# Kernel optimization log

Hardware: AMD Instinct MI355X
Metric: run time of the kernel (lower is better)

The kernel has to match this reference:

```python
import jax, jax.numpy as jnp
import numpy as np

N_NODES = 100000
N_EDGES = 1600000
H_FEATS = 128
OUT_CLASSES = 6


def setup_inputs() -> dict:
    key = jax.random.key(0)
    ks = jax.random.split(key, 9)
    h = jax.random.normal(ks[0], (N_NODES, H_FEATS), dtype=jnp.float32)
    src = jax.random.randint(ks[1], (N_EDGES,), 0, N_NODES)
    dst = jax.random.randint(ks[2], (N_EDGES,), 0, N_NODES)
    # torch nn.Linear convention: y = x @ W.T + b, W shape [out, in]
    W1 = jax.random.normal(ks[3], (64, 2 * H_FEATS), dtype=jnp.float32) * 0.05
    b1 = jax.random.normal(ks[4], (64,), dtype=jnp.float32) * 0.05
    W2 = jax.random.normal(ks[5], (32, 64), dtype=jnp.float32) * 0.05
    b2 = jax.random.normal(ks[6], (32,), dtype=jnp.float32) * 0.05
    W3 = jax.random.normal(ks[7], (OUT_CLASSES, 32), dtype=jnp.float32) * 0.05
    b3 = jax.random.normal(ks[8], (OUT_CLASSES,), dtype=jnp.float32) * 0.05
    return {"h": h, "src": src, "dst": dst, "W1": W1, "b1": b1,
            "W2": W2, "b2": b2, "W3": W3, "b3": b3}


def reference(h, src, dst, W1, b1, W2, b2, W3, b3):
    # Per-edge gather of src/dst node features, concat -> [E, 2*H]
    x = jnp.concatenate([h[src], h[dst]], axis=1)
    x = jax.nn.relu(x @ W1.T + b1)   # [E, 64]
    x = jax.nn.relu(x @ W2.T + b2)   # [E, 32]
    return x @ W3.T + b3             # [E, output_class]
```

## Files before the change

kernel.cpp:

```cpp
#include <hip/hip_runtime.h>
#include <hip/hip_bf16.h>
#include <stdint.h>


#define H 128

typedef short bf16x8 __attribute__((ext_vector_type(8)));
typedef float f32x4  __attribute__((ext_vector_type(4)));

__device__ __forceinline__ uint16_t f2bf(float f) {
    uint32_t u = __float_as_uint(f);
    return (uint16_t)((u + 0x7fffu + ((u >> 16) & 1u)) >> 16);
}

__device__ __forceinline__ uint32_t cvtpk(float lo, float hi) {
    uint32_t r;
    asm("v_cvt_pk_bf16_f32 %0, %1, %2" : "=v"(r) : "v"(lo), "v"(hi));
    return r;
}

__device__ __forceinline__ uint32_t bfadd2_relu(uint32_t a, uint32_t b) {
    float alo = __uint_as_float(a << 16);
    float ahi = __uint_as_float(a & 0xffff0000u);
    float blo = __uint_as_float(b << 16);
    float bhi = __uint_as_float(b & 0xffff0000u);
    float slo = fmaxf(alo + blo, 0.f);
    float shi = fmaxf(ahi + bhi, 0.f);
    return cvtpk(slo, shi);
}

__global__ void prep_weights(const float* __restrict__ W1,
                             const float* __restrict__ W2,
                             const float* __restrict__ W3,
                             uint16_t* __restrict__ Bfrag,
                             uint16_t* __restrict__ EFrag)
{
    int t = blockIdx.x * blockDim.x + threadIdx.x;
    int stride = gridDim.x * blockDim.x;
    for (int i = t; i < 4 * 8 * 64 * 8; i += stride) {
        int j    = i & 7;
        int lane = (i >> 3) & 63;
        int nt   = (i >> 9) & 7;
        int kt   = (i >> 12);
        int k = kt * 32 + (lane >> 4) * 8 + j;
        int n = nt * 16 + (lane & 15);
        float v = (n < 64) ? W1[n * 256 + k] : W1[(n - 64) * 256 + 128 + k];
        Bfrag[i] = f2bf(v);
    }
    for (int i = t; i < 5 * 64 * 8; i += stride) {
        int j    = i & 7;
        int lane = (i >> 3) & 63;
        int f    = i >> 9;
        uint16_t v;
        if (f < 4) {
            int kt = f >> 1, nt = f & 1;
            int k = kt * 32 + (lane >> 4) * 8 + j;
            int n = nt * 16 + (lane & 15);
            v = f2bf(W2[n * 64 + k]);
        } else {
            int k = (lane >> 4) * 8 + j;
            int n = lane & 15;
            v = (n < 6) ? f2bf(W3[n * 32 + k]) : (uint16_t)0;
        }
        EFrag[i] = v;
    }
}

__global__ void __launch_bounds__(256) node_gemm(
    const float* __restrict__ h,
    const uint16_t* __restrict__ Bfrag,
    const float* __restrict__ b1,
    uint16_t* __restrict__ pre, int N)
{
    const int wave = threadIdx.x >> 6;
    const int lane = threadIdx.x & 63;
    const int n0 = (blockIdx.x * 4 + wave) * 32;
    if (n0 >= N) return;

    const int m15  = lane & 15;
    const int quad = lane >> 4;

    bf16x8 hb[2][4];
#pragma unroll
    for (int t = 0; t < 2; t++) {
        int row = n0 + t * 16 + m15; if (row >= N) row = N - 1;
        const float* hrow = h + (size_t)row * H + quad * 8;
#pragma unroll
        for (int kt = 0; kt < 4; kt++) {
            float4 lo = *(const float4*)(hrow + kt * 32);
            float4 hi = *(const float4*)(hrow + kt * 32 + 4);
            union { bf16x8 v; uint32_t u[4]; } B;
            B.u[0] = cvtpk(lo.x, lo.y); B.u[1] = cvtpk(lo.z, lo.w);
            B.u[2] = cvtpk(hi.x, hi.y); B.u[3] = cvtpk(hi.z, hi.w);
            hb[t][kt] = B.v;
        }
    }

    const bool ok0 = (n0 + m15) < N;
    const bool ok1 = (n0 + 16 + m15) < N;
    uint16_t* prow0 = pre + (size_t)(n0 + m15) * H;
    uint16_t* prow1 = pre + (size_t)(n0 + 16 + m15) * H;

#pragma unroll
    for (int ct = 0; ct < 8; ct++) {
        f32x4 acc0 = {0.f, 0.f, 0.f, 0.f};
        f32x4 acc1 = {0.f, 0.f, 0.f, 0.f};
#pragma unroll
        for (int kt = 0; kt < 4; kt++) {
            bf16x8 afr = *(const bf16x8*)(Bfrag + ((size_t)(kt * 8 + ct) * 64 + lane) * 8);
            acc0 = __builtin_amdgcn_mfma_f32_16x16x32_bf16(afr, hb[0][kt], acc0, 0, 0, 0);
            acc1 = __builtin_amdgcn_mfma_f32_16x16x32_bf16(afr, hb[1][kt], acc1, 0, 0, 0);
        }
        float4 bv = {0.f, 0.f, 0.f, 0.f};
        if (ct < 4) bv = *(const float4*)(b1 + ct * 16 + quad * 4);
        const int off = ct * 16 + quad * 4;
        if (ok0) {
            uint32_t p0 = cvtpk(acc0[0] + bv.x, acc0[1] + bv.y);
            uint32_t p1 = cvtpk(acc0[2] + bv.z, acc0[3] + bv.w);
            *(uint2*)(prow0 + off) = uint2{p0, p1};
        }
        if (ok1) {
            uint32_t p0 = cvtpk(acc1[0] + bv.x, acc1[1] + bv.y);
            uint32_t p1 = cvtpk(acc1[2] + bv.z, acc1[3] + bv.w);
            *(uint2*)(prow1 + off) = uint2{p0, p1};
        }
    }
}

__global__ void __launch_bounds__(256) edge_mlp(
    const uint16_t* __restrict__ pre,
    const int* __restrict__ src, const int* __restrict__ dst,
    const uint16_t* __restrict__ EFrag,
    const float* __restrict__ b2, const float* __restrict__ b3,
    float* __restrict__ out, long E)
{
    __shared__ uint16_t zbuf[4][64 * 40];

    const int wave = threadIdx.x >> 6;
    const int lane = threadIdx.x & 63;
    const int m15  = lane & 15;
    const int quad = lane >> 4;
    uint16_t* zw = &zbuf[wave][0];

    bf16x8 bL2[4], bL3;
#pragma unroll
    for (int f = 0; f < 4; f++) bL2[f] = *(const bf16x8*)(EFrag + (f * 64 + lane) * 8);
    bL3 = *(const bf16x8*)(EFrag + (4 * 64 + lane) * 8);
    const float4 vb2a4 = *(const float4*)(b2 + quad * 4);
    const float4 vb2b4 = *(const float4*)(b2 + 16 + quad * 4);
    const float vb3  = (m15 < 6) ? b3[m15] : 0.f;

    const long e0 = (long)(blockIdx.x * 4 + wave) * 64;
    if (e0 >= E) return;

    const char* preb = (const char*)pre;
    uint32_t oa0, oa1, oa2, oa3, ob0, ob1, ob2, ob3;
    {
        long ea = e0 + m15;
        long eb = (ea + 16 < E) ? ea + 16 : E - 1;
        long ec = (ea + 32 < E) ? ea + 32 : E - 1;
        long ed = (ea + 48 < E) ? ea + 48 : E - 1;
        if (ea >= E) ea = E - 1;
        oa0 = (uint32_t)src[ea] * 256u + (uint32_t)quad * 16u;
        ob0 = (uint32_t)dst[ea] * 256u + 128u + (uint32_t)quad * 16u;
        oa1 = (uint32_t)src[eb] * 256u + (uint32_t)quad * 16u;
        ob1 = (uint32_t)dst[eb] * 256u + 128u + (uint32_t)quad * 16u;
        oa2 = (uint32_t)src[ec] * 256u + (uint32_t)quad * 16u;
        ob2 = (uint32_t)dst[ec] * 256u + 128u + (uint32_t)quad * 16u;
        oa3 = (uint32_t)src[ed] * 256u + (uint32_t)quad * 16u;
        ob3 = (uint32_t)dst[ed] * 256u + 128u + (uint32_t)quad * 16u;
    }
    uint4 a00 = *(const uint4*)(preb + oa0);
    uint4 a01 = *(const uint4*)(preb + oa0 + 64);
    uint4 b00 = *(const uint4*)(preb + ob0);
    uint4 b01 = *(const uint4*)(preb + ob0 + 64);
    uint4 a10 = *(const uint4*)(preb + oa1);
    uint4 a11 = *(const uint4*)(preb + oa1 + 64);
    uint4 b10 = *(const uint4*)(preb + ob1);
    uint4 b11 = *(const uint4*)(preb + ob1 + 64);
    uint4 a20 = *(const uint4*)(preb + oa2);
    uint4 a21 = *(const uint4*)(preb + oa2 + 64);
    uint4 b20 = *(const uint4*)(preb + ob2);
    uint4 b21 = *(const uint4*)(preb + ob2 + 64);
    uint4 a30 = *(const uint4*)(preb + oa3);
    uint4 a31 = *(const uint4*)(preb + oa3 + 64);
    uint4 b30 = *(const uint4*)(preb + ob3);
    uint4 b31 = *(const uint4*)(preb + ob3 + 64);

#define DO_SUBTILE(ST, UA0, UB0, UA1, UB1)                                        \
    {                                                                             \
        union { bf16x8 v; uint32_t u[4]; } A0, A1;                                \
        A0.u[0] = bfadd2_relu(UA0.x, UB0.x);                                      \
        A0.u[1] = bfadd2_relu(UA0.y, UB0.y);                                      \
        A0.u[2] = bfadd2_relu(UA0.z, UB0.z);                                      \
        A0.u[3] = bfadd2_relu(UA0.w, UB0.w);                                      \
        A1.u[0] = bfadd2_relu(UA1.x, UB1.x);                                      \
        A1.u[1] = bfadd2_relu(UA1.y, UB1.y);                                      \
        A1.u[2] = bfadd2_relu(UA1.z, UB1.z);                                      \
        A1.u[3] = bfadd2_relu(UA1.w, UB1.w);                                      \
        _Pragma("unroll")                                                         \
        for (int nt = 0; nt < 2; nt++) {                                          \
            f32x4 acc = {0.f, 0.f, 0.f, 0.f};                                     \
            acc = __builtin_amdgcn_mfma_f32_16x16x32_bf16(bL2[nt], A0.v, acc, 0, 0, 0); \
            acc = __builtin_amdgcn_mfma_f32_16x16x32_bf16(bL2[2 + nt], A1.v, acc, 0, 0, 0); \
            const float4 bv = nt ? vb2b4 : vb2a4;                                 \
            uint32_t p0 = cvtpk(fmaxf(acc[0] + bv.x, 0.f), fmaxf(acc[1] + bv.y, 0.f)); \
            uint32_t p1 = cvtpk(fmaxf(acc[2] + bv.z, 0.f), fmaxf(acc[3] + bv.w, 0.f)); \
            *(uint2*)(zw + ((ST) * 16 + m15) * 40 + nt * 16 + quad * 4) = uint2{p0, p1}; \
        }                                                                         \
    }

    DO_SUBTILE(0, a00, b00, a01, b01)
    DO_SUBTILE(1, a10, b10, a11, b11)
    DO_SUBTILE(2, a20, b20, a21, b21)
    DO_SUBTILE(3, a30, b30, a31, b31)
#undef DO_SUBTILE

#pragma unroll
    for (int st = 0; st < 4; st++) {
        bf16x8 a3 = *(const bf16x8*)(zw + (st * 16 + m15) * 40 + quad * 8);
        f32x4 o = {0.f, 0.f, 0.f, 0.f};
        o = __builtin_amdgcn_mfma_f32_16x16x32_bf16(a3, bL3, o, 0, 0, 0);
        if (m15 < 6) {
#pragma unroll
            for (int r = 0; r < 4; r++) {
                long e = e0 + st * 16 + quad * 4 + r;
                if (e < E) out[e * 6 + m15] = o[r] + vb3;
            }
        }
    }
}

extern "C" void kernel_launch(void* const* d_in, const int* in_sizes, int n_in,
                              void* d_out, int out_size, void* d_ws, size_t ws_size,
                              hipStream_t stream) {
    const float* h   = (const float*)d_in[0];
    const int*   src = (const int*)d_in[1];
    const int*   dst = (const int*)d_in[2];
    const float* W1  = (const float*)d_in[3];
    const float* b1  = (const float*)d_in[4];
    const float* W2  = (const float*)d_in[5];
    const float* b2  = (const float*)d_in[6];
    const float* W3  = (const float*)d_in[7];
    const float* b3  = (const float*)d_in[8];

    const int  N = in_sizes[0] / H;
    const long E = in_sizes[1];

    char* ws = (char*)d_ws;
    uint16_t* Bfrag = (uint16_t*)ws;
    uint16_t* EFrag = (uint16_t*)(ws + 64 * 1024);
    uint16_t* pre   = (uint16_t*)(ws + 128 * 1024);

    prep_weights<<<64, 256, 0, stream>>>(W1, W2, W3, Bfrag, EFrag);
    node_gemm<<<(N + 127) / 128, 256, 0, stream>>>(h, Bfrag, b1, pre, N);
    const int eblocks = (int)((E + 255) / 256);
    edge_mlp<<<eblocks, 256, 0, stream>>>(pre, src, dst, EFrag, b2, b3,
                                          (float*)d_out, E);
}
```

Before: 190.0 us.

## Replace LDS staging with ds_bpermute and double edges per wave in edge MLP

The layer-2 to layer-3 handoff used to go through a per-wave shared memory buffer. It now moves the packed bf16 activations between lanes with ds_bpermute, which removes the LDS allocation and the store/load round trip. Each wave now handles 128 edges instead of 64, issuing 32 gather loads up front for more memory-level parallelism, and the kernel gets a launch-bounds occupancy hint of 8. The larger in-flight register set risks spills or lower occupancy under the new bound, and fewer blocks are launched.

```diff
diff --git a/kernel.cpp b/kernel.cpp
--- a/kernel.cpp
+++ b/kernel.cpp
@@ -127,20 +127,17 @@
     }
 }
 
-__global__ void __launch_bounds__(256) edge_mlp(
+__global__ void __launch_bounds__(256, 8) edge_mlp(
     const uint16_t* __restrict__ pre,
     const int* __restrict__ src, const int* __restrict__ dst,
     const uint16_t* __restrict__ EFrag,
     const float* __restrict__ b2, const float* __restrict__ b3,
     float* __restrict__ out, long E)
 {
-    __shared__ uint16_t zbuf[4][64 * 40];
-
     const int wave = threadIdx.x >> 6;
     const int lane = threadIdx.x & 63;
     const int m15  = lane & 15;
     const int quad = lane >> 4;
-    uint16_t* zw = &zbuf[wave][0];
 
     bf16x8 bL2[4], bL3;
 #pragma unroll
@@ -150,77 +147,70 @@
     const float4 vb2b4 = *(const float4*)(b2 + 16 + quad * 4);
     const float vb3  = (m15 < 6) ? b3[m15] : 0.f;
 
-    const long e0 = (long)(blockIdx.x * 4 + wave) * 64;
+    const long e0 = (long)(blockIdx.x * 4 + wave) * 128;
     if (e0 >= E) return;
 
     const char* preb = (const char*)pre;
-    uint32_t oa0, oa1, oa2, oa3, ob0, ob1, ob2, ob3;
-    {
-        long ea = e0 + m15;
-        long eb = (ea + 16 < E) ? ea + 16 : E - 1;
-        long ec = (ea + 32 < E) ? ea + 32 : E - 1;
-        long ed = (ea + 48 < E) ? ea + 48 : E - 1;
-        if (ea >= E) ea = E - 1;
-        oa0 = (uint32_t)src[ea] * 256u + (uint32_t)quad * 16u;
-        ob0 = (uint32_t)dst[ea] * 256u + 128u + (uint32_t)quad * 16u;
-        oa1 = (uint32_t)src[eb] * 256u + (uint32_t)quad * 16u;
-        ob1 = (uint32_t)dst[eb] * 256u + 128u + (uint32_t)quad * 16u;
-        oa2 = (uint32_t)src[ec] * 256u + (uint32_t)quad * 16u;
-        ob2 = (uint32_t)dst[ec] * 256u + 128u + (uint32_t)quad * 16u;
-        oa3 = (uint32_t)src[ed] * 256u + (uint32_t)quad * 16u;
-        ob3 = (uint32_t)dst[ed] * 256u + 128u + (uint32_t)quad * 16u;
-    }
-    uint4 a00 = *(const uint4*)(preb + oa0);
-    uint4 a01 = *(const uint4*)(preb + oa0 + 64);
-    uint4 b00 = *(const uint4*)(preb + ob0);
-    uint4 b01 = *(const uint4*)(preb + ob0 + 64);
-    uint4 a10 = *(const uint4*)(preb + oa1);
-    uint4 a11 = *(const uint4*)(preb + oa1 + 64);
-    uint4 b10 = *(const uint4*)(preb + ob1);
-    uint4 b11 = *(const uint4*)(preb + ob1 + 64);
-    uint4 a20 = *(const uint4*)(preb + oa2);
-    uint4 a21 = *(const uint4*)(preb + oa2 + 64);
-    uint4 b20 = *(const uint4*)(preb + ob2);
-    uint4 b21 = *(const uint4*)(preb + ob2 + 64);
-    uint4 a30 = *(const uint4*)(preb + oa3);
-    uint4 a31 = *(const uint4*)(preb + oa3 + 64);
-    uint4 b30 = *(const uint4*)(preb + ob3);
-    uint4 b31 = *(const uint4*)(preb + ob3 + 64);
-
-#define DO_SUBTILE(ST, UA0, UB0, UA1, UB1)                                        \
-    {                                                                             \
-        union { bf16x8 v; uint32_t u[4]; } A0, A1;                                \
-        A0.u[0] = bfadd2_relu(UA0.x, UB0.x);                                      \
-        A0.u[1] = bfadd2_relu(UA0.y, UB0.y);                                      \
-        A0.u[2] = bfadd2_relu(UA0.z, UB0.z);                                      \
-        A0.u[3] = bfadd2_relu(UA0.w, UB0.w);                                      \
-        A1.u[0] = bfadd2_relu(UA1.x, UB1.x);                                      \
-        A1.u[1] = bfadd2_relu(UA1.y, UB1.y);                                      \
-        A1.u[2] = bfadd2_relu(UA1.z, UB1.z);                                      \
-        A1.u[3] = bfadd2_relu(UA1.w, UB1.w);                                      \
-        _Pragma("unroll")                                                         \
-        for (int nt = 0; nt < 2; nt++) {                                          \
-            f32x4 acc = {0.f, 0.f, 0.f, 0.f};                                     \
-            acc = __builtin_amdgcn_mfma_f32_16x16x32_bf16(bL2[nt], A0.v, acc, 0, 0, 0); \
-            acc = __builtin_amdgcn_mfma_f32_16x16x32_bf16(bL2[2 + nt], A1.v, acc, 0, 0, 0); \
-            const float4 bv = nt ? vb2b4 : vb2a4;                                 \
-            uint32_t p0 = cvtpk(fmaxf(acc[0] + bv.x, 0.f), fmaxf(acc[1] + bv.y, 0.f)); \
-            uint32_t p1 = cvtpk(fmaxf(acc[2] + bv.z, 0.f), fmaxf(acc[3] + bv.w, 0.f)); \
-            *(uint2*)(zw + ((ST) * 16 + m15) * 40 + nt * 16 + quad * 4) = uint2{p0, p1}; \
-        }                                                                         \
-    }
-
-    DO_SUBTILE(0, a00, b00, a01, b01)
-    DO_SUBTILE(1, a10, b10, a11, b11)
-    DO_SUBTILE(2, a20, b20, a21, b21)
-    DO_SUBTILE(3, a30, b30, a31, b31)
-#undef DO_SUBTILE
-
-#pragma unroll
-    for (int st = 0; st < 4; st++) {
-        bf16x8 a3 = *(const bf16x8*)(zw + (st * 16 + m15) * 40 + quad * 8);
+    uint32_t oa[8], ob[8];
+#pragma unroll
+    for (int st = 0; st < 8; st++) {
+        long e = e0 + st * 16 + m15;
+        if (e >= E) e = E - 1;
+        oa[st] = (uint32_t)src[e] * 256u + (uint32_t)quad * 16u;
+        ob[st] = (uint32_t)dst[e] * 256u + 128u + (uint32_t)quad * 16u;
+    }
+    uint4 ga[8][2], gb[8][2];
+#pragma unroll
+    for (int st = 0; st < 8; st++) {
+        ga[st][0] = *(const uint4*)(preb + oa[st]);
+        ga[st][1] = *(const uint4*)(preb + oa[st] + 64);
+        gb[st][0] = *(const uint4*)(preb + ob[st]);
+        gb[st][1] = *(const uint4*)(preb + ob[st] + 64);
+    }
+
+    const int addrA = (((quad & 1) << 5) | m15) << 2;
+    const int addrB = addrA + 64;
+    const bool hiNT = (quad >= 2);
+
+#pragma unroll
+    for (int st = 0; st < 8; st++) {
+        union { bf16x8 v; uint32_t u[4]; } A0, A1;
+        A0.u[0] = bfadd2_relu(ga[st][0].x, gb[st][0].x);
+        A0.u[1] = bfadd2_relu(ga[st][0].y, gb[st][0].y);
+        A0.u[2] = bfadd2_relu(ga[st][0].z, gb[st][0].z);
+        A0.u[3] = bfadd2_relu(ga[st][0].w, gb[st][0].w);
+        A1.u[0] = bfadd2_relu(ga[st][1].x, gb[st][1].x);
+        A1.u[1] = bfadd2_relu(ga[st][1].y, gb[st][1].y);
+        A1.u[2] = bfadd2_relu(ga[st][1].z, gb[st][1].z);
+        A1.u[3] = bfadd2_relu(ga[st][1].w, gb[st][1].w);
+
+        uint32_t pk[2][2];
+#pragma unroll
+        for (int nt = 0; nt < 2; nt++) {
+            f32x4 acc = {0.f, 0.f, 0.f, 0.f};
+            acc = __builtin_amdgcn_mfma_f32_16x16x32_bf16(bL2[nt],     A0.v, acc, 0, 0, 0);
+            acc = __builtin_amdgcn_mfma_f32_16x16x32_bf16(bL2[2 + nt], A1.v, acc, 0, 0, 0);
+            const float4 bv = nt ? vb2b4 : vb2a4;
+            pk[nt][0] = cvtpk(fmaxf(acc[0] + bv.x, 0.f), fmaxf(acc[1] + bv.y, 0.f));
+            pk[nt][1] = cvtpk(fmaxf(acc[2] + bv.z, 0.f), fmaxf(acc[3] + bv.w, 0.f));
+        }
+
+        int d0n0 = __builtin_amdgcn_ds_bpermute(addrA, (int)pk[0][0]);
+        int d1n0 = __builtin_amdgcn_ds_bpermute(addrA, (int)pk[0][1]);
+        int d2n0 = __builtin_amdgcn_ds_bpermute(addrB, (int)pk[0][0]);
+        int d3n0 = __builtin_amdgcn_ds_bpermute(addrB, (int)pk[0][1]);
+        int d0n1 = __builtin_amdgcn_ds_bpermute(addrA, (int)pk[1][0]);
+        int d1n1 = __builtin_amdgcn_ds_bpermute(addrA, (int)pk[1][1]);
+        int d2n1 = __builtin_amdgcn_ds_bpermute(addrB, (int)pk[1][0]);
+        int d3n1 = __builtin_amdgcn_ds_bpermute(addrB, (int)pk[1][1]);
+        union { bf16x8 v; int u[4]; } A3;
+        A3.u[0] = hiNT ? d0n1 : d0n0;
+        A3.u[1] = hiNT ? d1n1 : d1n0;
+        A3.u[2] = hiNT ? d2n1 : d2n0;
+        A3.u[3] = hiNT ? d3n1 : d3n0;
+
         f32x4 o = {0.f, 0.f, 0.f, 0.f};
-        o = __builtin_amdgcn_mfma_f32_16x16x32_bf16(a3, bL3, o, 0, 0, 0);
+        o = __builtin_amdgcn_mfma_f32_16x16x32_bf16(A3.v, bL3, o, 0, 0, 0);
         if (m15 < 6) {
 #pragma unroll
             for (int r = 0; r < 4; r++) {
@@ -254,7 +244,7 @@
 
     prep_weights<<<64, 256, 0, stream>>>(W1, W2, W3, Bfrag, EFrag);
     node_gemm<<<(N + 127) / 128, 256, 0, stream>>>(h, Bfrag, b1, pre, N);
-    const int eblocks = (int)((E + 255) / 256);
+    const int eblocks = (int)((E + 511) / 512);
     edge_mlp<<<eblocks, 256, 0, stream>>>(pre, src, dst, EFrag, b2, b3,
                                           (float*)d_out, E);
 }
```

New measurement: 319.0 us. +67.9%, slower.
